# Kernel optimization log

Measured on AMD Instinct MI355X. Metric: run time of the kernel, lower is better.

Reference implementation:

```python
import jax, jax.numpy as jnp
import numpy as np

B, D, N = 128, 768, 256  # batch, feature dim (hard-coded 768 in module), neighbors


def setup_inputs() -> dict:
    key = jax.random.key(0)
    k1, k2, k3, k4, k5, k6, k7 = jax.random.split(key, 7)
    s = 1.0 / np.sqrt(D)  # torch Linear default init scale
    return {
        "h_v": jax.random.normal(k1, (B, D, N), dtype=jnp.float32),
        "h_w": jax.random.normal(k2, (B, D, N), dtype=jnp.float32),
        "e_vw": jax.random.normal(k3, (B, D, N), dtype=jnp.float32),
        "We": jax.random.uniform(k4, (D, D), jnp.float32, -s, s),
        "be": jax.random.uniform(k5, (D,), jnp.float32, -s, s),
        "Ww": jax.random.uniform(k6, (D, D), jnp.float32, -s, s),
        "bw": jax.random.uniform(k7, (D,), jnp.float32, -s, s),
    }


def reference(h_v, h_w, e_vw, We, be, Ww, bw):
    # m_linear: message[:, :, n] = Linear_e(e_vw[:, :, n]) + Linear_w(h_w[:, :, n])
    # Fused as two batched GEMMs over all neighbors at once. h_v is unused (as in source).
    msg = (
        jnp.einsum("od,bdn->bon", We, e_vw)
        + jnp.einsum("od,bdn->bon", Ww, h_w)
        + (be + bw)[None, :, None]
    )
    return msg  # [B, 768, N]
```

## Files before the change

kernel.cpp:

```cpp
#include <hip/hip_runtime.h>


#define DD   768
#define NCOL 256
#define KTOT 1536
#define BM   192
#define BN   256
#define BK   64
#define NIT  24

typedef __bf16 bf16;
typedef __attribute__((ext_vector_type(8))) __bf16 bf16x8;
typedef __attribute__((ext_vector_type(4))) float f32x4;
typedef __attribute__((ext_vector_type(4))) unsigned int u32x4;

__device__ __forceinline__ int swz(int row, int kb) {
  return row * 128 + (kb ^ (((row ^ (row >> 3)) & 7) << 4));
}

__global__ void prep_w(const float* __restrict__ We, const float* __restrict__ Ww,
                       unsigned short* __restrict__ Wfrag) {
  int i = blockIdx.x * blockDim.x + threadIdx.x;
  int lane = i & 63;
  int r = i >> 6;
  int M = r % 12;  r /= 12;
  int s = r & 1;   r >>= 1;
  int T = r % 24;
  int mt = r / 24;
  int o = mt * 192 + M * 16 + (lane & 15);
  int k = T * 64 + s * 32 + (lane >> 4) * 8;
  const float* src = (k < DD) ? (We + (size_t)o * DD + k)
                              : (Ww + (size_t)o * DD + (k - DD));
  f32x4 v0 = *(const f32x4*)src;
  f32x4 v1 = *(const f32x4*)(src + 4);
  union { bf16 h8[8]; u32x4 q; } u;
  u.h8[0]=(bf16)v0[0]; u.h8[1]=(bf16)v0[1]; u.h8[2]=(bf16)v0[2]; u.h8[3]=(bf16)v0[3];
  u.h8[4]=(bf16)v1[0]; u.h8[5]=(bf16)v1[1]; u.h8[6]=(bf16)v1[2]; u.h8[7]=(bf16)v1[3];
  *(u32x4*)(Wfrag + (size_t)i * 8) = u.q;
}

__global__ __launch_bounds__(512, 2)
void msg_kernel(const float* __restrict__ h_w, const float* __restrict__ e_vw,
                const unsigned short* __restrict__ Wfrag,
                const float* __restrict__ be, const float* __restrict__ bw,
                float* __restrict__ out) {
  __shared__ __align__(16) unsigned char smem[2 * 32768 + 768];
  float* bias_s = (float*)(smem + 65536);

  const int tid = threadIdx.x;
  const int p = blockIdx.x;
  const int slot = p >> 3;
  const int bb = (p & 7) * 16 + (slot >> 2);
  const int mt = slot & 3;
  const int bm0 = mt * 192;

  if (tid < 192) bias_s[tid] = be[bm0 + tid] + bw[bm0 + tid];

  const int nq = tid & 63, kk = tid >> 6;
  const size_t xofs = (size_t)bb * DD * NCOL + (size_t)(kk * 8) * NCOL + nq * 4;
  const float* pE = e_vw + xofs;
  const float* pH = h_w + xofs;
  int wBo[4];
  #pragma unroll
  for (int j = 0; j < 4; ++j) wBo[j] = swz(4 * nq + j, kk * 16);

  f32x4 bR[8];

  auto issueB = [&](int T) {
    const float* q = (T < 12) ? (pE + (size_t)T * BK * NCOL)
                              : (pH + (size_t)(T - 12) * BK * NCOL);
    #pragma unroll
    for (int i = 0; i < 8; ++i) bR[i] = *(const f32x4*)(q + (size_t)i * NCOL);
  };
  auto storeB = [&](int buf) {
    unsigned char* base = smem + buf * 32768;
    #pragma unroll
    for (int j = 0; j < 4; ++j) {
      union { bf16 h8[8]; u32x4 q; } u;
      #pragma unroll
      for (int i = 0; i < 8; ++i) u.h8[i] = (bf16)bR[i][j];
      *(u32x4*)(base + wBo[j]) = u.q;
    }
  };

  const int lane = tid & 63, wid = tid >> 6;
  const int wm = wid >> 2, wn = wid & 3;
  const int lr = lane & 15, qk = (lane >> 4) * 16;
  const int wm6 = wm * 6;
  f32x4 acc[6][4] = {};

  const unsigned short* pW = Wfrag + ((size_t)mt * 24 * 2 * 12 * 64 + (size_t)lane) * 8;
  bf16x8 af[12];

  auto loadA = [&](int T) {
    #pragma unroll
    for (int s = 0; s < 2; ++s)
      #pragma unroll
      for (int m = 0; m < 6; ++m)
        af[s * 6 + m] =
            *(const bf16x8*)(pW + (size_t)(((T * 2 + s) * 12 + wm6 + m) * 64) * 8);
  };

  issueB(0);
  storeB(0);
  loadA(0);
  issueB(1);
  asm volatile("s_waitcnt lgkmcnt(0)" ::: "memory");
  __builtin_amdgcn_s_barrier();

  for (int t = 0; t < NIT; ++t) {
    const int c = t & 1;
    const unsigned char* bB = smem + c * 32768;
    bf16x8 bfv0[4], bfv1[4];

    #pragma unroll
    for (int n = 0; n < 4; ++n)
      bfv0[n] = *(const bf16x8*)(bB + swz(wn * 64 + n * 16 + lr, qk));
    #pragma unroll
    for (int n = 0; n < 4; ++n)
      bfv1[n] = *(const bf16x8*)(bB + swz(wn * 64 + n * 16 + lr, 64 + qk));

    #pragma unroll
    for (int m = 0; m < 6; ++m)
      #pragma unroll
      for (int n = 0; n < 4; ++n)
        acc[m][n] = __builtin_amdgcn_mfma_f32_16x16x32_bf16(af[m], bfv0[n], acc[m][n], 0, 0, 0);

    if (t < NIT - 1) storeB(c ^ 1);

    #pragma unroll
    for (int m = 0; m < 6; ++m)
      #pragma unroll
      for (int n = 0; n < 4; ++n)
        acc[m][n] = __builtin_amdgcn_mfma_f32_16x16x32_bf16(af[6 + m], bfv1[n], acc[m][n], 0, 0, 0);

    if (t < NIT - 1) loadA(t + 1);
    if (t < NIT - 2) issueB(t + 2);

    asm volatile("s_waitcnt lgkmcnt(0)" ::: "memory");
    __builtin_amdgcn_s_barrier();
  }

  float* po = out + (size_t)bb * DD * NCOL;
  const int g4 = (lane >> 4) * 4;
  #pragma unroll
  for (int m = 0; m < 6; ++m) {
    const int r0 = wm * 96 + m * 16 + g4;
    #pragma unroll
    for (int n = 0; n < 4; ++n) {
      const int col = wn * 64 + n * 16 + lr;
      #pragma unroll
      for (int j = 0; j < 4; ++j)
        po[(size_t)(bm0 + r0 + j) * NCOL + col] = acc[m][n][j] + bias_s[r0 + j];
    }
  }
}

extern "C" void kernel_launch(void* const* d_in, const int* in_sizes, int n_in,
                              void* d_out, int out_size, void* d_ws, size_t ws_size,
                              hipStream_t stream) {
  const float* h_w  = (const float*)d_in[1];
  const float* e_vw = (const float*)d_in[2];
  const float* We   = (const float*)d_in[3];
  const float* be   = (const float*)d_in[4];
  const float* Ww   = (const float*)d_in[5];
  const float* bw   = (const float*)d_in[6];
  float* out = (float*)d_out;
  unsigned short* Wfrag = (unsigned short*)d_ws;

  prep_w<<<dim3(576), 256, 0, stream>>>(We, Ww, Wfrag);
  msg_kernel<<<dim3(512), 512, 0, stream>>>(h_w, e_vw, Wfrag, be, bw, out);
}
```

Baseline: 126.1 us.

## Shrink GEMM tiles to 128x128 with 256-thread blocks and split N

Changes the output tile from 192x256 to 128x128 and halves the block to 256 threads (4 waves, 2x2). The grid grows from 512 to 1536 blocks, with a new mapping that splits the neighbor dimension in two and spreads batches across XCDs. The weight fragment layout in prep_w changes to match. The goal is better load balance and occupancy across the 256 CUs. In exchange, each element of the activation and weight tiles is reused fewer times and global and LDS traffic per FLOP rises.

```diff
diff --git a/kernel.cpp b/kernel.cpp
--- a/kernel.cpp
+++ b/kernel.cpp
@@ -4,8 +4,8 @@
 #define DD   768
 #define NCOL 256
 #define KTOT 1536
-#define BM   192
-#define BN   256
+#define BM   128
+#define BN   128
 #define BK   64
 #define NIT  24
 
@@ -23,11 +23,11 @@
   int i = blockIdx.x * blockDim.x + threadIdx.x;
   int lane = i & 63;
   int r = i >> 6;
-  int M = r % 12;  r /= 12;
-  int s = r & 1;   r >>= 1;
-  int T = r % 24;
-  int mt = r / 24;
-  int o = mt * 192 + M * 16 + (lane & 15);
+  int M = r & 7;
+  int s = (r >> 3) & 1;
+  int T = (r >> 4) % 24;
+  int mt = r / 384;
+  int o = mt * 128 + M * 16 + (lane & 15);
   int k = T * 64 + s * 32 + (lane >> 4) * 8;
   const float* src = (k < DD) ? (We + (size_t)o * DD + k)
                               : (Ww + (size_t)o * DD + (k - DD));
@@ -39,30 +39,33 @@
   *(u32x4*)(Wfrag + (size_t)i * 8) = u.q;
 }
 
-__global__ __launch_bounds__(512, 2)
+__global__ __launch_bounds__(256, 2)
 void msg_kernel(const float* __restrict__ h_w, const float* __restrict__ e_vw,
                 const unsigned short* __restrict__ Wfrag,
                 const float* __restrict__ be, const float* __restrict__ bw,
                 float* __restrict__ out) {
-  __shared__ __align__(16) unsigned char smem[2 * 32768 + 768];
-  float* bias_s = (float*)(smem + 65536);
+  __shared__ __align__(16) unsigned char smem[2 * 16384 + 512];
+  float* bias_s = (float*)(smem + 32768);
 
   const int tid = threadIdx.x;
   const int p = blockIdx.x;
-  const int slot = p >> 3;
-  const int bb = (p & 7) * 16 + (slot >> 2);
-  const int mt = slot & 3;
-  const int bm0 = mt * 192;
+  const int xcd = p & 7;
+  const int i6 = p >> 3;
+  const int mt = i6 % 6;
+  const int g = (i6 / 6) * 8 + xcd;
+  const int bb = g >> 1;
+  const int bn0 = (g & 1) * BN;
+  const int bm0 = mt * BM;
 
-  if (tid < 192) bias_s[tid] = be[bm0 + tid] + bw[bm0 + tid];
+  if (tid < BM) bias_s[tid] = be[bm0 + tid] + bw[bm0 + tid];
 
-  const int nq = tid & 63, kk = tid >> 6;
-  const size_t xofs = (size_t)bb * DD * NCOL + (size_t)(kk * 8) * NCOL + nq * 4;
+  const int nq4 = (tid & 31) * 4, kk = tid >> 5;
+  const size_t xofs = (size_t)bb * DD * NCOL + (size_t)(kk * 8) * NCOL + bn0 + nq4;
   const float* pE = e_vw + xofs;
   const float* pH = h_w + xofs;
   int wBo[4];
   #pragma unroll
-  for (int j = 0; j < 4; ++j) wBo[j] = swz(4 * nq + j, kk * 16);
+  for (int j = 0; j < 4; ++j) wBo[j] = swz(nq4 + j, kk * 16);
 
   f32x4 bR[8];
 
@@ -73,7 +76,7 @@
     for (int i = 0; i < 8; ++i) bR[i] = *(const f32x4*)(q + (size_t)i * NCOL);
   };
   auto storeB = [&](int buf) {
-    unsigned char* base = smem + buf * 32768;
+    unsigned char* base = smem + buf * 16384;
     #pragma unroll
     for (int j = 0; j < 4; ++j) {
       union { bf16 h8[8]; u32x4 q; } u;
@@ -84,21 +87,20 @@
   };
 
   const int lane = tid & 63, wid = tid >> 6;
-  const int wm = wid >> 2, wn = wid & 3;
+  const int wm = wid >> 1, wn = wid & 1;
   const int lr = lane & 15, qk = (lane >> 4) * 16;
-  const int wm6 = wm * 6;
-  f32x4 acc[6][4] = {};
+  f32x4 acc[4][4] = {};
 
-  const unsigned short* pW = Wfrag + ((size_t)mt * 24 * 2 * 12 * 64 + (size_t)lane) * 8;
-  bf16x8 af[12];
+  const unsigned short* pW = Wfrag + ((size_t)mt * 24 * 2 * 8 * 64 + (size_t)lane) * 8;
+  bf16x8 af[8];
 
   auto loadA = [&](int T) {
     #pragma unroll
     for (int s = 0; s < 2; ++s)
       #pragma unroll
-      for (int m = 0; m < 6; ++m)
-        af[s * 6 + m] =
-            *(const bf16x8*)(pW + (size_t)(((T * 2 + s) * 12 + wm6 + m) * 64) * 8);
+      for (int m = 0; m < 4; ++m)
+        af[s * 4 + m] =
+            *(const bf16x8*)(pW + (size_t)(((T * 2 + s) * 8 + wm * 4 + m) * 64) * 8);
   };
 
   issueB(0);
@@ -110,7 +112,7 @@
 
   for (int t = 0; t < NIT; ++t) {
     const int c = t & 1;
-    const unsigned char* bB = smem + c * 32768;
+    const unsigned char* bB = smem + c * 16384;
     bf16x8 bfv0[4], bfv1[4];
 
     #pragma unroll
@@ -121,7 +123,7 @@
       bfv1[n] = *(const bf16x8*)(bB + swz(wn * 64 + n * 16 + lr, 64 + qk));
 
     #pragma unroll
-    for (int m = 0; m < 6; ++m)
+    for (int m = 0; m < 4; ++m)
       #pragma unroll
       for (int n = 0; n < 4; ++n)
         acc[m][n] = __builtin_amdgcn_mfma_f32_16x16x32_bf16(af[m], bfv0[n], acc[m][n], 0, 0, 0);
@@ -129,10 +131,10 @@
     if (t < NIT - 1) storeB(c ^ 1);
 
     #pragma unroll
-    for (int m = 0; m < 6; ++m)
+    for (int m = 0; m < 4; ++m)
       #pragma unroll
       for (int n = 0; n < 4; ++n)
-        acc[m][n] = __builtin_amdgcn_mfma_f32_16x16x32_bf16(af[6 + m], bfv1[n], acc[m][n], 0, 0, 0);
+        acc[m][n] = __builtin_amdgcn_mfma_f32_16x16x32_bf16(af[4 + m], bfv1[n], acc[m][n], 0, 0, 0);
 
     if (t < NIT - 1) loadA(t + 1);
     if (t < NIT - 2) issueB(t + 2);
@@ -144,11 +146,11 @@
   float* po = out + (size_t)bb * DD * NCOL;
   const int g4 = (lane >> 4) * 4;
   #pragma unroll
-  for (int m = 0; m < 6; ++m) {
-    const int r0 = wm * 96 + m * 16 + g4;
+  for (int m = 0; m < 4; ++m) {
+    const int r0 = wm * 64 + m * 16 + g4;
     #pragma unroll
     for (int n = 0; n < 4; ++n) {
-      const int col = wn * 64 + n * 16 + lr;
+      const int col = bn0 + wn * 64 + n * 16 + lr;
       #pragma unroll
       for (int j = 0; j < 4; ++j)
         po[(size_t)(bm0 + r0 + j) * NCOL + col] = acc[m][n][j] + bias_s[r0 + j];
@@ -169,5 +171,5 @@
   unsigned short* Wfrag = (unsigned short*)d_ws;
 
   prep_w<<<dim3(576), 256, 0, stream>>>(We, Ww, Wfrag);
-  msg_kernel<<<dim3(512), 512, 0, stream>>>(h_w, e_vw, Wfrag, be, bw, out);
+  msg_kernel<<<dim3(1536), 256, 0, stream>>>(h_w, e_vw, Wfrag, be, bw, out);
 }
```

Result: slower. 148.1 us (+17.4%).

## Stage weight fragments through LDS via async global_load_lds DMA

Applied to the files above, without the earlier changes.

Weight fragments are no longer loaded straight from global memory into registers each iteration. They are now copied asynchronously into double-buffered LDS with global_load_lds and read back as fragments, and the manual vmcnt waits are adjusted to match. The B tile uses a new fragment-ordered LDS layout with a rotated store order in place of the XOR swizzle, and the B global load is issued earlier in the loop. This is meant to cut register pressure and global-load latency on the A operand. In exchange it uses about 115 KB of LDS per block, which may limit occupancy to one block per CU.

```diff
diff --git a/kernel.cpp b/kernel.cpp
--- a/kernel.cpp
+++ b/kernel.cpp
@@ -3,19 +3,23 @@
 
 #define DD   768
 #define NCOL 256
-#define KTOT 1536
 #define BM   192
 #define BN   256
 #define BK   64
 #define NIT  24
+#define ABYTES 24576
+#define BUFSZ  57344
 
 typedef __bf16 bf16;
 typedef __attribute__((ext_vector_type(8))) __bf16 bf16x8;
 typedef __attribute__((ext_vector_type(4))) float f32x4;
 typedef __attribute__((ext_vector_type(4))) unsigned int u32x4;
 
-__device__ __forceinline__ int swz(int row, int kb) {
-  return row * 128 + (kb ^ (((row ^ (row >> 3)) & 7) << 4));
+__device__ __forceinline__ void dma16(const void* g, const void* lds_generic) {
+  __builtin_amdgcn_global_load_lds(
+      (const __attribute__((address_space(1))) unsigned int*)(unsigned long long)g,
+      (__attribute__((address_space(3))) unsigned int*)(unsigned int)(unsigned long long)lds_generic,
+      16, 0, 0);
 }
 
 __global__ void prep_w(const float* __restrict__ We, const float* __restrict__ Ww,
@@ -44,8 +48,8 @@
                 const unsigned short* __restrict__ Wfrag,
                 const float* __restrict__ be, const float* __restrict__ bw,
                 float* __restrict__ out) {
-  __shared__ __align__(16) unsigned char smem[2 * 32768 + 768];
-  float* bias_s = (float*)(smem + 65536);
+  __shared__ __align__(16) unsigned char smem[2 * BUFSZ + 768];
+  float* bias_s = (float*)(smem + 2 * BUFSZ);
 
   const int tid = threadIdx.x;
   const int p = blockIdx.x;
@@ -56,13 +60,26 @@
 
   if (tid < 192) bias_s[tid] = be[bm0 + tid] + bw[bm0 + tid];
 
+  const int lane = tid & 63, wid = tid >> 6;
+  const int wm = wid >> 2, wn = wid & 3;
+  const int wm6 = wm * 6;
+
+  const unsigned short* pWt = Wfrag + (size_t)(mt * 24) * 24 * 64 * 8;
+  auto dmaA = [&](int buf, int T) {
+    const unsigned short* tb = pWt + (size_t)T * 24 * 64 * 8;
+    #pragma unroll
+    for (int jj = 0; jj < 3; ++jj) {
+      const int f = wid * 3 + jj;
+      dma16(tb + (size_t)(f * 64 + lane) * 8, smem + buf * BUFSZ + f * 1024);
+    }
+  };
+
   const int nq = tid & 63, kk = tid >> 6;
+  const int sB = kk >> 2, kc = kk & 3, nb4 = nq >> 2, nl = nq & 3;
   const size_t xofs = (size_t)bb * DD * NCOL + (size_t)(kk * 8) * NCOL + nq * 4;
   const float* pE = e_vw + xofs;
   const float* pH = h_w + xofs;
-  int wBo[4];
-  #pragma unroll
-  for (int j = 0; j < 4; ++j) wBo[j] = swz(4 * nq + j, kk * 16);
+  const int cbase = (sB * 16 + nb4) * 64 + kc * 16 + nl * 4;
 
   f32x4 bR[8];
 
@@ -73,75 +90,75 @@
     for (int i = 0; i < 8; ++i) bR[i] = *(const f32x4*)(q + (size_t)i * NCOL);
   };
   auto storeB = [&](int buf) {
-    unsigned char* base = smem + buf * 32768;
+    unsigned char* base = smem + buf * BUFSZ + ABYTES;
     #pragma unroll
-    for (int j = 0; j < 4; ++j) {
+    for (int i = 0; i < 4; ++i) {
+      const int j = (i + nb4) & 3;
       union { bf16 h8[8]; u32x4 q; } u;
       #pragma unroll
-      for (int i = 0; i < 8; ++i) u.h8[i] = (bf16)bR[i][j];
-      *(u32x4*)(base + wBo[j]) = u.q;
+      for (int r = 0; r < 8; ++r) u.h8[r] = (bf16)bR[r][j];
+      *(u32x4*)(base + (size_t)(cbase + j) * 16) = u.q;
     }
   };
 
-  const int lane = tid & 63, wid = tid >> 6;
-  const int wm = wid >> 2, wn = wid & 3;
-  const int lr = lane & 15, qk = (lane >> 4) * 16;
-  const int wm6 = wm * 6;
   f32x4 acc[6][4] = {};
 
-  const unsigned short* pW = Wfrag + ((size_t)mt * 24 * 2 * 12 * 64 + (size_t)lane) * 8;
-  bf16x8 af[12];
-
-  auto loadA = [&](int T) {
-    #pragma unroll
-    for (int s = 0; s < 2; ++s)
-      #pragma unroll
-      for (int m = 0; m < 6; ++m)
-        af[s * 6 + m] =
-            *(const bf16x8*)(pW + (size_t)(((T * 2 + s) * 12 + wm6 + m) * 64) * 8);
-  };
-
   issueB(0);
+  dmaA(0, 0);
+  __builtin_amdgcn_sched_barrier(0);
   storeB(0);
-  loadA(0);
   issueB(1);
-  asm volatile("s_waitcnt lgkmcnt(0)" ::: "memory");
+  asm volatile("s_waitcnt vmcnt(8) lgkmcnt(0)" ::: "memory");
   __builtin_amdgcn_s_barrier();
 
   for (int t = 0; t < NIT; ++t) {
     const int c = t & 1;
-    const unsigned char* bB = smem + c * 32768;
-    bf16x8 bfv0[4], bfv1[4];
+    const unsigned char* bA = smem + c * BUFSZ;
+    const unsigned char* bB = bA + ABYTES;
 
+    if (t < NIT - 1) dmaA(c ^ 1, t + 1);
+    __builtin_amdgcn_sched_barrier(0);
+
+    bf16x8 af0[6], bfv0[4], af1[6], bfv1[4];
+    #pragma unroll
+    for (int m = 0; m < 6; ++m)
+      af0[m] = *(const bf16x8*)(bA + (size_t)((wm6 + m) * 64 + lane) * 16);
     #pragma unroll
     for (int n = 0; n < 4; ++n)
-      bfv0[n] = *(const bf16x8*)(bB + swz(wn * 64 + n * 16 + lr, qk));
-    #pragma unroll
-    for (int n = 0; n < 4; ++n)
-      bfv1[n] = *(const bf16x8*)(bB + swz(wn * 64 + n * 16 + lr, 64 + qk));
+      bfv0[n] = *(const bf16x8*)(bB + (size_t)((wn * 4 + n) * 64 + lane) * 16);
 
     #pragma unroll
     for (int m = 0; m < 6; ++m)
       #pragma unroll
       for (int n = 0; n < 4; ++n)
-        acc[m][n] = __builtin_amdgcn_mfma_f32_16x16x32_bf16(af[m], bfv0[n], acc[m][n], 0, 0, 0);
+        acc[m][n] = __builtin_amdgcn_mfma_f32_16x16x32_bf16(af0[m], bfv0[n], acc[m][n], 0, 0, 0);
+
+    #pragma unroll
+    for (int m = 0; m < 6; ++m)
+      af1[m] = *(const bf16x8*)(bA + (size_t)((12 + wm6 + m) * 64 + lane) * 16);
+    #pragma unroll
+    for (int n = 0; n < 4; ++n)
+      bfv1[n] = *(const bf16x8*)(bB + (size_t)((16 + wn * 4 + n) * 64 + lane) * 16);
 
     if (t < NIT - 1) storeB(c ^ 1);
+    if (t < NIT - 2) issueB(t + 2);
 
     #pragma unroll
     for (int m = 0; m < 6; ++m)
       #pragma unroll
       for (int n = 0; n < 4; ++n)
-        acc[m][n] = __builtin_amdgcn_mfma_f32_16x16x32_bf16(af[6 + m], bfv1[n], acc[m][n], 0, 0, 0);
+        acc[m][n] = __builtin_amdgcn_mfma_f32_16x16x32_bf16(af1[m], bfv1[n], acc[m][n], 0, 0, 0);
 
-    if (t < NIT - 1) loadA(t + 1);
-    if (t < NIT - 2) issueB(t + 2);
-
-    asm volatile("s_waitcnt lgkmcnt(0)" ::: "memory");
+    if (t < NIT - 2) {
+      asm volatile("s_waitcnt vmcnt(8) lgkmcnt(0)" ::: "memory");
+    } else {
+      asm volatile("s_waitcnt vmcnt(0) lgkmcnt(0)" ::: "memory");
+    }
     __builtin_amdgcn_s_barrier();
   }
 
   float* po = out + (size_t)bb * DD * NCOL;
+  const int lr = lane & 15;
   const int g4 = (lane >> 4) * 4;
   #pragma unroll
   for (int m = 0; m < 6; ++m) {
```

Result: slower. 436.5 us (+246.1%).
